# Optimization experiments

Hardware: AMD Instinct MI355X
Metric: run time of the kernel (lower is better)

## Reference

```python
import jax, jax.numpy as jnp
import numpy as np

HO, WO = 64, 64
SHARPNESS = 150.0


def _stereographic_grid(ho, wo):
    # Matches create_normal_grid(..., 'stereographic'); torch.meshgrid 'ij':
    # v varies over rows (ho), u over cols (wo).
    v, u = np.meshgrid(np.arange(ho), np.arange(wo), indexing='ij')
    p = 4.0 * ((u + 0.5) / wo - 0.5)
    q = -4.0 * ((v + 0.5) / ho - 0.5)
    d = 1.0 + p ** 2 + q ** 2
    z = -(-1.0 + p ** 2 + q ** 2) / d
    m = (z > 0.0).astype(np.float32)
    x = 2.0 * p / d * m
    y = 2.0 * q / d * m
    z = z * m
    return np.stack([x, y, z], axis=-1).reshape(-1, 3).astype(np.float32)  # [ho*wo,3]


_GRID = _stereographic_grid(HO, WO)
_IDX = np.nonzero(np.any(_GRID != 0, axis=-1))[0]  # static valid-query indices [N]
_QN = _GRID[_IDX]  # [N,3]


def setup_inputs() -> dict:
    key = jax.random.key(0)
    k1, k2, k3 = jax.random.split(key, 3)
    bs, c, h, w = 2, 64, 192, 192
    in_fea_map = jax.random.normal(k1, (bs, c, h, w), dtype=jnp.float32)
    nrm = jax.random.normal(k2, (bs, 3, h, w), dtype=jnp.float32)
    in_normal_map = nrm / (jnp.linalg.norm(nrm, axis=1, keepdims=True) + 1e-8)
    in_mask_map = (jax.random.uniform(k3, (bs, 1, h, w)) > 0.2).astype(jnp.float32)
    log_query_norm = jnp.full((1,), np.log(SHARPNESS), dtype=jnp.float32)
    return {"in_fea_map": in_fea_map, "in_normal_map": in_normal_map,
            "in_mask_map": in_mask_map, "log_query_norm": log_query_norm}


def reference(in_fea_map, in_normal_map, in_mask_map, log_query_norm):
    bs, c, h, w = in_fea_map.shape
    hw = h * w
    qn = jnp.asarray(_QN, dtype=in_fea_map.dtype)  # [N,3] static valid queries
    vals = in_fea_map.reshape(bs, c, hw).transpose(0, 2, 1)       # [bs,HW,c]
    key_n = in_normal_map.reshape(bs, 3, hw)                       # [bs,3,HW]
    cos = jnp.einsum('nd,bdm->bnm', qn, key_n)                     # [bs,N,HW]
    dps = cos / np.float32(np.sqrt(3.0))
    dps = dps - jnp.max(dps, axis=-1, keepdims=True)
    w_ = jnp.exp(jnp.exp(log_query_norm) * dps)                    # dropout in eval = identity
    w_ = w_ * in_mask_map.reshape(bs, 1, hw)
    weights = w_ / (jnp.sum(w_, axis=-1, keepdims=True) + 1e-9)    # [bs,N,HW]
    mapped = weights @ vals                                        # [bs,N,c]
    mapped = jnp.concatenate([jnp.broadcast_to(qn, (bs,) + qn.shape), mapped], axis=-1)
    # variance map over last 3 feature channels
    mean = mapped[..., -3:]
    sq_mean = weights @ (vals[..., -3:] ** 2)
    var = jnp.sum(sq_mean - mean ** 2, axis=-1, keepdims=True)
    mapped = jnp.concatenate([var, mapped], axis=-1)
    # cosine map
    rm_cos = jnp.sum(weights * cos, axis=-1, keepdims=True)
    mapped = jnp.concatenate([rm_cos, mapped], axis=-1)            # [bs,N,c+5]
    C = mapped.shape[-1]
    out = jnp.zeros((bs, HO * WO, C), mapped.dtype).at[:, _IDX, :].set(mapped)
    return out.transpose(0, 2, 1).reshape(bs, C, HO, WO)
```

## Files before the change

kernel.cpp:

```cpp
#include <hip/hip_runtime.h>
#include <hip/hip_bf16.h>
#include <cstdint>
#include <cstddef>

#define HW 36864
#define QT 64
#define NCHA 69

constexpr bool is_valid_px(int v, int u) {
  int a = 2 * u - 63, b = 2 * v - 63;
  return a * a + b * b < 1024;
}
constexpr int count_valid() {
  int n = 0;
  for (int v = 0; v < 64; ++v)
    for (int u = 0; u < 64; ++u)
      if (is_valid_px(v, u)) ++n;
  return n;
}
constexpr int NV  = count_valid();
constexpr int NQT = (NV + QT - 1) / QT;
constexpr int NQP = NQT * QT;
constexpr int PLANE = 2 * NQP * NCHA;

struct QTab {
  short idx[NQP];
  short rank[4096];
};
constexpr QTab make_qtab() {
  QTab t{};
  int n = 0;
  for (int p = 0; p < 4096; ++p) {
    int v = p >> 6, u = p & 63;
    if (is_valid_px(v, u)) { t.idx[n] = (short)p; t.rank[p] = (short)n; ++n; }
    else t.rank[p] = -1;
  }
  for (int i = n; i < NQP; ++i) t.idx[i] = -1;
  return t;
}
__constant__ QTab g_qtab = make_qtab();

typedef short short8 __attribute__((ext_vector_type(8)));
typedef float f32x4  __attribute__((ext_vector_type(4)));

__device__ __forceinline__ unsigned short f2b(float f) {
  unsigned int u = __float_as_uint(f);
  u += 0x7FFFu + ((u >> 16) & 1u);
  return (unsigned short)(u >> 16);
}
__device__ __forceinline__ ushort2 f2b2(float a, float b) {
  __hip_bfloat162 h = __float22bfloat162_rn(make_float2(a, b));
  return *(ushort2*)&h;
}
__device__ __forceinline__ ushort4 f2b4(float4 v) {
  ushort4 r;
  *(ushort2*)&r.x = f2b2(v.x, v.y);
  *(ushort2*)&r.z = f2b2(v.z, v.w);
  return r;
}
__device__ __forceinline__ void pix2qn(int pix, float& x, float& y, float& z) {
  x = 0.f; y = 0.f; z = 0.f;
  if (pix >= 0) {
    int v = pix >> 6, u = pix & 63;
    float p = (float)(2 * u - 63) * (1.0f / 32.0f);
    float q = -(float)(2 * v - 63) * (1.0f / 32.0f);
    float d = 1.0f + p * p + q * q;
    x = 2.0f * p / d; y = 2.0f * q / d; z = (1.0f - p * p - q * q) / d;
  }
}


template<int KSC>
__global__ __launch_bounds__(256, 4) void partial_kernel(
    const float* __restrict__ fea,
    const float* __restrict__ nrm,
    const float* __restrict__ msk,
    const float* __restrict__ lqn,
    float* __restrict__ part)
{
  constexpr int SLICE  = HW / KSC;
  constexpr int NCHUNK = SLICE / 64;

  __shared__ __align__(16) unsigned short v_s[2][80][72];
  __shared__ __align__(16) float nrm4_s[2][64][4];

  const int bx  = blockIdx.x;
  const int cls = bx & 7;
  const int r0  = bx >> 3;
  const int qt  = r0 % NQT;
  const int sh  = r0 / NQT;
  const int s   = sh * 8 + cls;
  const int b   = s / KSC;
  const int ks  = s % KSC;

  const int t    = threadIdx.x;
  const int wv   = t >> 6;
  const int Mh   = wv & 1;
  const int kko  = (wv >> 1) * 32;
  const int l    = t & 63;
  const int lq   = l >> 4;
  const int mrow = l & 15;

  const float Cc = __expf(lqn[0]) * 0.57735026919f;

  float qx[2], qy[2], qz[2];
  pix2qn(g_qtab.idx[qt * QT + 32 * Mh + mrow],      qx[0], qy[0], qz[0]);
  pix2qn(g_qtab.idx[qt * QT + 32 * Mh + 16 + mrow], qx[1], qy[1], qz[1]);

  if (t < 160) {
    int row = 70 + (t >> 4);
    int p4  = (t & 15) * 4;
    unsigned short c = (row == 70) ? (unsigned short)0x3F80 : (unsigned short)0;
    ushort4 cv; cv.x = c; cv.y = c; cv.z = c; cv.w = c;
    *(ushort4*)&v_s[0][row][p4] = cv;
    *(ushort4*)&v_s[1][row][p4] = cv;
  }

  const size_t base_f = (size_t)b * 64 * HW;
  const size_t base_n = (size_t)b * 3 * HW;
  const size_t base_m = (size_t)b * HW;

  const int chb = t >> 4;
  const int px4 = (t & 15) * 4;
  const int arr = t >> 6;
  const int pxp = 32 * (l >> 5) + 4 * (l & 7) + ((l >> 3) & 3);

  f32x4 acc[2][5];
  #pragma unroll
  for (int h = 0; h < 2; ++h)
    #pragma unroll
    for (int nt = 0; nt < 5; ++nt) acc[h][nt] = (f32x4)(0.0f);

  float4 pf[4];
  float pn = 0.f, pm = 0.f;

  auto load_chunk = [&](int ck) {
    int m0 = ks * SLICE + ck * 64;
    #pragma unroll
    for (int i = 0; i < 4; ++i)
      pf[i] = *(const float4*)(fea + base_f + (size_t)(chb + 16 * i) * HW + (size_t)(m0 + px4));
    if (arr < 3) pn = nrm[base_n + (size_t)arr * HW + (size_t)(m0 + l)];
    else         pm = msk[base_m + (size_t)(m0 + l)];
  };
  auto store_chunk = [&](int buf) {
    #pragma unroll
    for (int i = 0; i < 4; ++i) {
      int ch = chb + 16 * i;
      float4 fv = pf[i];
      *(ushort4*)&v_s[buf][ch][px4] = f2b4(fv);
      if (ch >= 61) {
        float4 sq = make_float4(fv.x * fv.x, fv.y * fv.y, fv.z * fv.z, fv.w * fv.w);
        *(ushort4*)&v_s[buf][ch + 3][px4] = f2b4(sq);
      }
    }
    if (arr < 3) {
      v_s[buf][67 + arr][l] = f2b(pn);
      nrm4_s[buf][pxp][arr] = Cc * pn;
    } else {
      nrm4_s[buf][pxp][3] = -Cc + (pm > 0.5f ? 0.f : -2000.f);
    }
  };

  load_chunk(0);
  store_chunk(0);
  __syncthreads();

  for (int ck = 0; ck < NCHUNK; ++ck) {
    const int buf = ck & 1;
    if (ck + 1 < NCHUNK) load_chunk(ck + 1);

    float e0[8], e1[8];
    #pragma unroll
    for (int j = 0; j < 8; ++j) {
      const float4 nv = *(const float4*)&nrm4_s[buf][kko + 4 * j + lq][0];
      float t0 = fmaf(qx[0], nv.x, fmaf(qy[0], nv.y, fmaf(qz[0], nv.z, nv.w)));
      float t1 = fmaf(qx[1], nv.x, fmaf(qy[1], nv.y, fmaf(qz[1], nv.z, nv.w)));
      e0[j] = __expf(t0);
      e1[j] = __expf(t1);
    }
    short8 a0, a1;
    #pragma unroll
    for (int p = 0; p < 4; ++p) {
      ushort2 p0 = f2b2(e0[2 * p], e0[2 * p + 1]);
      ushort2 p1 = f2b2(e1[2 * p], e1[2 * p + 1]);
      a0[2 * p] = (short)p0.x; a0[2 * p + 1] = (short)p0.y;
      a1[2 * p] = (short)p1.x; a1[2 * p + 1] = (short)p1.y;
    }
    #pragma unroll
    for (int nt = 0; nt < 5; ++nt) {
      short8 bb = *(const short8*)&v_s[buf][16 * nt + mrow][kko + 8 * lq];
      acc[0][nt] = __builtin_amdgcn_mfma_f32_16x16x32_bf16(a0, bb, acc[0][nt], 0, 0, 0);
      acc[1][nt] = __builtin_amdgcn_mfma_f32_16x16x32_bf16(a1, bb, acc[1][nt], 0, 0, 0);
    }

    if (ck + 1 < NCHUNK) {
      store_chunk(buf ^ 1);
      __syncthreads();
    }
  }

  __syncthreads();
  float* scr = (float*)&v_s[0][0][0];
  float* exs = scr + 64 * 80;

  if (kko) {
    #pragma unroll
    for (int h = 0; h < 2; ++h)
      #pragma unroll
      for (int nt = 0; nt < 5; ++nt)
        #pragma unroll
        for (int rr = 0; rr < 4; ++rr) {
          int qloc = 32 * Mh + 16 * h + 4 * lq + rr;
          scr[qloc * 80 + 16 * nt + mrow] = acc[h][nt][rr];
        }
  }
  __syncthreads();
  const size_t pbase = (size_t)ks * PLANE + ((size_t)b * NQP + (size_t)(qt * QT)) * NCHA;
  if (!kko) {
    #pragma unroll
    for (int h = 0; h < 2; ++h) {
      #pragma unroll
      for (int nt = 0; nt < 5; ++nt)
        #pragma unroll
        for (int rr = 0; rr < 4; ++rr) {
          int qloc = 32 * Mh + 16 * h + 4 * lq + rr;
          acc[h][nt][rr] += scr[qloc * 80 + 16 * nt + mrow];
        }
      #pragma unroll
      for (int nt = 0; nt < 4; ++nt)
        #pragma unroll
        for (int rr = 0; rr < 4; ++rr) {
          int qloc = 32 * Mh + 16 * h + 4 * lq + rr;
          part[pbase + (size_t)qloc * NCHA + (size_t)(16 * nt + mrow)] = acc[h][nt][rr];
        }
      if (mrow < 7) {
        #pragma unroll
        for (int rr = 0; rr < 4; ++rr)
          exs[(32 * Mh + 16 * h + 4 * lq + rr) * 9 + mrow] = acc[h][4][rr];
      }
    }
  }
  __syncthreads();
  if (t < 64) {
    float gx, gy, gz;
    pix2qn(g_qtab.idx[qt * QT + t], gx, gy, gz);
    const float* E = exs + t * 9;
    float swc = gx * E[3] + gy * E[4] + gz * E[5];
    size_t o = pbase + (size_t)t * NCHA;
    part[o + 64] = E[0];
    part[o + 65] = E[1];
    part[o + 66] = E[2];
    part[o + 67] = swc;
    part[o + 68] = E[6];
  }
}

#define NFIN (2 * NQT * 8)
#define NTAIL (2 * NFIN)

__global__ __launch_bounds__(256) void finalize_kernel(
    const float* __restrict__ part,
    float* __restrict__ out,
    int ksc)
{
  const int blk = blockIdx.x;
  const int t   = threadIdx.x;

  if (blk < NFIN) {
    __shared__ float sm[8][NCHA];
    const int b   = blk / (NQT * 8);
    const int rem = blk % (NQT * 8);
    const int qt  = rem >> 3;
    const int qr  = rem & 7;
    const int q0  = qt * QT + qr * 8;

    const size_t colbase = ((size_t)b * NQP + (size_t)q0) * NCHA;
    for (int i = t; i < 8 * NCHA; i += 256) {
      float sv = 0.f;
      const size_t off = colbase + (size_t)i;
      #pragma unroll 8
      for (int k = 0; k < ksc; ++k) sv += part[(size_t)k * PLANE + off];
      sm[0][i] = sv;
    }
    __syncthreads();

    for (int i = t; i < 8 * NCHA; i += 256) {
      const int ql = i / NCHA;
      const int oc = i % NCHA;
      const int pix = g_qtab.idx[q0 + ql];
      if (pix < 0) continue;
      const float* A = sm[ql];
      const float inv = 1.0f / (A[68] + 1e-9f);
      float gx, gy, gz;
      pix2qn(pix, gx, gy, gz);
      float val;
      if (oc == 0)      val = A[67] * inv;
      else if (oc == 1) {
        val = 0.f;
        #pragma unroll
        for (int j = 0; j < 3; ++j) {
          float m  = A[61 + j] * inv;
          float sq = A[64 + j] * inv;
          val += sq - m * m;
        }
      }
      else if (oc == 2) val = gx;
      else if (oc == 3) val = gy;
      else if (oc == 4) val = gz;
      else              val = A[oc - 5] * inv;
      out[((size_t)b * NCHA + (size_t)oc) * 4096 + pix] = val;
    }
  } else {
    const int start = (blk - NFIN) * 256 + t;
    const int strd  = (NTAIL - NFIN) * 256;
    const int TOT   = 2 * NCHA * 4096;
    for (int i = start; i < TOT; i += strd) {
      if (g_qtab.rank[i & 4095] < 0) out[i] = 0.0f;
    }
  }
}

extern "C" void kernel_launch(void* const* d_in, const int* in_sizes, int n_in,
                              void* d_out, int out_size, void* d_ws, size_t ws_size,
                              hipStream_t stream) {
  const float* fea = (const float*)d_in[0];
  const float* nrm = (const float*)d_in[1];
  const float* msk = (const float*)d_in[2];
  const float* lqn = (const float*)d_in[3];
  float* part = (float*)d_ws;
  float* out  = (float*)d_out;

  const size_t need64 = (size_t)PLANE * 64 * sizeof(float);
  const size_t need32 = (size_t)PLANE * 32 * sizeof(float);
  if (ws_size >= need64) {
    partial_kernel<64><<<dim3(2 * 64 * NQT), 256, 0, stream>>>(fea, nrm, msk, lqn, part);
    finalize_kernel<<<dim3(NTAIL), 256, 0, stream>>>(part, out, 64);
  } else if (ws_size >= need32) {
    partial_kernel<32><<<dim3(2 * 32 * NQT), 256, 0, stream>>>(fea, nrm, msk, lqn, part);
    finalize_kernel<<<dim3(NTAIL), 256, 0, stream>>>(part, out, 32);
  } else {
    partial_kernel<16><<<dim3(2 * 16 * NQT), 256, 0, stream>>>(fea, nrm, msk, lqn, part);
    finalize_kernel<<<dim3(NTAIL), 256, 0, stream>>>(part, out, 16);
  }
}
```

Measured before the change: 118.9 us.

## Precompute bf16 value matrix and scaled normals in a separate prep kernel

After: 117.3 us. No clear change (-1.3%).

```diff
diff --git a/kernel.cpp b/kernel.cpp
--- a/kernel.cpp
+++ b/kernel.cpp
@@ -6,6 +6,7 @@
 #define HW 36864
 #define QT 64
 #define NCHA 69
+#define NCHK 576
 
 constexpr bool is_valid_px(int v, int u) {
   int a = 2 * u - 63, b = 2 * v - 63;
@@ -22,6 +23,11 @@
 constexpr int NQT = (NV + QT - 1) / QT;
 constexpr int NQP = NQT * QT;
 constexpr int PLANE = 2 * NQP * NCHA;
+
+constexpr size_t BM_SHORTS  = (size_t)2 * NCHK * 80 * 64;
+constexpr size_t BM_BYTES   = BM_SHORTS * 2;
+constexpr size_t NV_BYTES   = (size_t)2 * HW * 4 * 4;
+constexpr size_t PART_OFF   = BM_BYTES + NV_BYTES;
 
 struct QTab {
   short idx[NQP];
@@ -52,12 +58,6 @@
   __hip_bfloat162 h = __float22bfloat162_rn(make_float2(a, b));
   return *(ushort2*)&h;
 }
-__device__ __forceinline__ ushort4 f2b4(float4 v) {
-  ushort4 r;
-  *(ushort2*)&r.x = f2b2(v.x, v.y);
-  *(ushort2*)&r.z = f2b2(v.z, v.w);
-  return r;
-}
 __device__ __forceinline__ void pix2qn(int pix, float& x, float& y, float& z) {
   x = 0.f; y = 0.f; z = 0.f;
   if (pix >= 0) {
@@ -69,13 +69,66 @@
   }
 }
 
-
-template<int KSC>
-__global__ __launch_bounds__(256, 4) void partial_kernel(
+#define PREP_BM_BLKS 2880
+#define PREP_NV_BLKS 288
+
+__global__ __launch_bounds__(256) void prep_kernel(
     const float* __restrict__ fea,
     const float* __restrict__ nrm,
     const float* __restrict__ msk,
     const float* __restrict__ lqn,
+    unsigned short* __restrict__ Bm,
+    float* __restrict__ nv)
+{
+  const float Cc = __expf(lqn[0]) * 0.57735026919f;
+  if (blockIdx.x < PREP_BM_BLKS) {
+    int gid = blockIdx.x * 256 + threadIdx.x;
+    int g   = gid & 7;
+    int row = (gid >> 3) % 80;
+    int chk = ((gid >> 3) / 80) % NCHK;
+    int b   = gid / (8 * 80 * NCHK);
+    int px0 = chk * 64 + g * 8;
+    float v[8];
+    if (row < 64) {
+      const float* p = fea + ((size_t)b * 64 + row) * HW + px0;
+      #pragma unroll
+      for (int i = 0; i < 8; ++i) v[i] = p[i];
+    } else if (row < 67) {
+      const float* p = fea + ((size_t)b * 64 + (61 + row - 64)) * HW + px0;
+      #pragma unroll
+      for (int i = 0; i < 8; ++i) { float x = p[i]; v[i] = x * x; }
+    } else if (row < 70) {
+      const float* p = nrm + ((size_t)b * 3 + (row - 67)) * HW + px0;
+      #pragma unroll
+      for (int i = 0; i < 8; ++i) v[i] = p[i];
+    } else {
+      float c = (row == 70) ? 1.0f : 0.0f;
+      #pragma unroll
+      for (int i = 0; i < 8; ++i) v[i] = c;
+    }
+    short8 o;
+    #pragma unroll
+    for (int p2 = 0; p2 < 4; ++p2) {
+      ushort2 pr = f2b2(v[2 * p2], v[2 * p2 + 1]);
+      o[2 * p2] = (short)pr.x; o[2 * p2 + 1] = (short)pr.y;
+    }
+    *(short8*)&Bm[(((size_t)b * NCHK + chk) * 80 + row) * 64 + g * 8] = o;
+  } else {
+    int p = (blockIdx.x - PREP_BM_BLKS) * 256 + threadIdx.x;
+    int b = p / HW, px = p % HW;
+    float nx = nrm[((size_t)b * 3 + 0) * HW + px];
+    float ny = nrm[((size_t)b * 3 + 1) * HW + px];
+    float nz = nrm[((size_t)b * 3 + 2) * HW + px];
+    float mk = msk[(size_t)b * HW + px];
+    float bias = -Cc + (mk > 0.5f ? 0.f : -2000.f);
+    *(float4*)&nv[(size_t)p * 4] = make_float4(Cc * nx, Cc * ny, Cc * nz, bias);
+  }
+}
+
+template<int KSC>
+__global__ __launch_bounds__(256, 4) void partial_kernel(
+    const unsigned short* __restrict__ Bm,
+    const float* __restrict__ nv,
     float* __restrict__ part)
 {
   constexpr int SLICE  = HW / KSC;
@@ -101,28 +154,13 @@
   const int lq   = l >> 4;
   const int mrow = l & 15;
 
-  const float Cc = __expf(lqn[0]) * 0.57735026919f;
-
   float qx[2], qy[2], qz[2];
   pix2qn(g_qtab.idx[qt * QT + 32 * Mh + mrow],      qx[0], qy[0], qz[0]);
   pix2qn(g_qtab.idx[qt * QT + 32 * Mh + 16 + mrow], qx[1], qy[1], qz[1]);
 
-  if (t < 160) {
-    int row = 70 + (t >> 4);
-    int p4  = (t & 15) * 4;
-    unsigned short c = (row == 70) ? (unsigned short)0x3F80 : (unsigned short)0;
-    ushort4 cv; cv.x = c; cv.y = c; cv.z = c; cv.w = c;
-    *(ushort4*)&v_s[0][row][p4] = cv;
-    *(ushort4*)&v_s[1][row][p4] = cv;
-  }
-
-  const size_t base_f = (size_t)b * 64 * HW;
-  const size_t base_n = (size_t)b * 3 * HW;
-  const size_t base_m = (size_t)b * HW;
-
-  const int chb = t >> 4;
-  const int px4 = (t & 15) * 4;
-  const int arr = t >> 6;
+  const int g0r = t >> 3,          g0c = (t & 7) * 8;
+  const int g1r = (t + 256) >> 3,  g1c = g0c;
+  const int g2r = (t + 512) >> 3;
   const int pxp = 32 * (l >> 5) + 4 * (l & 7) + ((l >> 3) & 3);
 
   f32x4 acc[2][5];
@@ -131,34 +169,22 @@
     #pragma unroll
     for (int nt = 0; nt < 5; ++nt) acc[h][nt] = (f32x4)(0.0f);
 
-  float4 pf[4];
-  float pn = 0.f, pm = 0.f;
+  short8 pB[3];
+  float4 pnv;
 
   auto load_chunk = [&](int ck) {
-    int m0 = ks * SLICE + ck * 64;
-    #pragma unroll
-    for (int i = 0; i < 4; ++i)
-      pf[i] = *(const float4*)(fea + base_f + (size_t)(chb + 16 * i) * HW + (size_t)(m0 + px4));
-    if (arr < 3) pn = nrm[base_n + (size_t)arr * HW + (size_t)(m0 + l)];
-    else         pm = msk[base_m + (size_t)(m0 + l)];
+    int chkAbs = ks * NCHUNK + ck;
+    const unsigned short* src = Bm + ((size_t)b * NCHK + chkAbs) * (80 * 64);
+    pB[0] = *(const short8*)(src + (size_t)(t)       * 8);
+    pB[1] = *(const short8*)(src + (size_t)(t + 256) * 8);
+    if (t < 128) pB[2] = *(const short8*)(src + (size_t)(t + 512) * 8);
+    if (t < 64)  pnv = *(const float4*)&nv[((size_t)b * HW + chkAbs * 64 + l) * 4];
   };
   auto store_chunk = [&](int buf) {
-    #pragma unroll
-    for (int i = 0; i < 4; ++i) {
-      int ch = chb + 16 * i;
-      float4 fv = pf[i];
-      *(ushort4*)&v_s[buf][ch][px4] = f2b4(fv);
-      if (ch >= 61) {
-        float4 sq = make_float4(fv.x * fv.x, fv.y * fv.y, fv.z * fv.z, fv.w * fv.w);
-        *(ushort4*)&v_s[buf][ch + 3][px4] = f2b4(sq);
-      }
-    }
-    if (arr < 3) {
-      v_s[buf][67 + arr][l] = f2b(pn);
-      nrm4_s[buf][pxp][arr] = Cc * pn;
-    } else {
-      nrm4_s[buf][pxp][3] = -Cc + (pm > 0.5f ? 0.f : -2000.f);
-    }
+    *(short8*)&v_s[buf][g0r][g0c] = pB[0];
+    *(short8*)&v_s[buf][g1r][g1c] = pB[1];
+    if (t < 128) *(short8*)&v_s[buf][g2r][g0c] = pB[2];
+    if (t < 64)  *(float4*)&nrm4_s[buf][pxp][0] = pnv;
   };
 
   load_chunk(0);
@@ -172,9 +198,9 @@
     float e0[8], e1[8];
     #pragma unroll
     for (int j = 0; j < 8; ++j) {
-      const float4 nv = *(const float4*)&nrm4_s[buf][kko + 4 * j + lq][0];
-      float t0 = fmaf(qx[0], nv.x, fmaf(qy[0], nv.y, fmaf(qz[0], nv.z, nv.w)));
-      float t1 = fmaf(qx[1], nv.x, fmaf(qy[1], nv.y, fmaf(qz[1], nv.z, nv.w)));
+      const float4 nvv = *(const float4*)&nrm4_s[buf][kko + 4 * j + lq][0];
+      float t0 = fmaf(qx[0], nvv.x, fmaf(qy[0], nvv.y, fmaf(qz[0], nvv.z, nvv.w)));
+      float t1 = fmaf(qx[1], nvv.x, fmaf(qy[1], nvv.y, fmaf(qz[1], nvv.z, nvv.w)));
       e0[j] = __expf(t0);
       e1[j] = __expf(t1);
     }
@@ -327,19 +353,24 @@
   const float* nrm = (const float*)d_in[1];
   const float* msk = (const float*)d_in[2];
   const float* lqn = (const float*)d_in[3];
-  float* part = (float*)d_ws;
+  unsigned short* Bm = (unsigned short*)d_ws;
+  float* nv   = (float*)((char*)d_ws + BM_BYTES);
+  float* part = (float*)((char*)d_ws + PART_OFF);
   float* out  = (float*)d_out;
 
-  const size_t need64 = (size_t)PLANE * 64 * sizeof(float);
-  const size_t need32 = (size_t)PLANE * 32 * sizeof(float);
+  prep_kernel<<<dim3(PREP_BM_BLKS + PREP_NV_BLKS), 256, 0, stream>>>(
+      fea, nrm, msk, lqn, Bm, nv);
+
+  const size_t need64 = PART_OFF + (size_t)PLANE * 64 * sizeof(float);
+  const size_t need32 = PART_OFF + (size_t)PLANE * 32 * sizeof(float);
   if (ws_size >= need64) {
-    partial_kernel<64><<<dim3(2 * 64 * NQT), 256, 0, stream>>>(fea, nrm, msk, lqn, part);
+    partial_kernel<64><<<dim3(2 * 64 * NQT), 256, 0, stream>>>(Bm, nv, part);
     finalize_kernel<<<dim3(NTAIL), 256, 0, stream>>>(part, out, 64);
   } else if (ws_size >= need32) {
-    partial_kernel<32><<<dim3(2 * 32 * NQT), 256, 0, stream>>>(fea, nrm, msk, lqn, part);
+    partial_kernel<32><<<dim3(2 * 32 * NQT), 256, 0, stream>>>(Bm, nv, part);
     finalize_kernel<<<dim3(NTAIL), 256, 0, stream>>>(part, out, 32);
   } else {
-    partial_kernel<16><<<dim3(2 * 16 * NQT), 256, 0, stream>>>(fea, nrm, msk, lqn, part);
+    partial_kernel<16><<<dim3(2 * 16 * NQT), 256, 0, stream>>>(Bm, nv, part);
     finalize_kernel<<<dim3(NTAIL), 256, 0, stream>>>(part, out, 16);
   }
 }
```
